# Kernel tuning notes

Hardware: AMD Instinct MI355X
Metric: run time of the kernel (lower is better)

The kernel has to match this reference:

```python
import jax, jax.numpy as jnp
import numpy as np

NQ = 10          # qubits per register
DIM = 2 ** NQ    # 1024 amplitudes
N_CLS = 10       # canonical images (one per class)
N = 16384        # batch of samples
IMG = 28 * 28    # 784 pixels, zero-padded to DIM


def setup_inputs() -> dict:
    key = jax.random.key(0)
    k1, k2, k3 = jax.random.split(key, 3)
    z_re = jax.random.normal(k1, (N, DIM), dtype=jnp.float32)
    z_im = jax.random.normal(k2, (N, DIM), dtype=jnp.float32)
    # inputs are quantum states -> L2-normalize the complex vectors
    nrm = jnp.sqrt(jnp.sum(z_re * z_re + z_im * z_im, axis=1, keepdims=True))
    z_re = z_re / nrm
    z_im = z_im / nrm
    canon = jax.random.uniform(k3, (N_CLS, 1, 28, 28), dtype=jnp.float32)
    return {"z_re": z_re, "z_im": z_im, "canon": canon}


def reference(z_re, z_im, canon):
    # reshape_norm_padding: flatten, zero-pad to 2^nq, L2-normalize (real amplitudes)
    ref = canon.reshape(N_CLS, IMG)
    ref = jnp.pad(ref, ((0, 0), (0, DIM - IMG)))                  # [C, DIM]
    ref = ref / jnp.linalg.norm(ref, axis=1, keepdims=True)
    # Swap test: <Z_anc> = |<val|ref>|^2. ref is real, so with val = z_re + i*z_im:
    #   <val|ref> = (z_re @ ref^T) - i*(z_im @ ref^T)
    s_re = jnp.einsum('nd,cd->nc', z_re, ref)                     # [N, C]
    s_im = jnp.einsum('nd,cd->nc', z_im, ref)                     # [N, C]
    return s_re * s_re + s_im * s_im                              # [N, C] float32
```

## Files before the change

kernel.cpp:

```cpp
#include <hip/hip_runtime.h>

#define NQ    10
#define DIM   1024
#define N_CLS 10
#define NROWS 16384
#define IMG   784

#define ROWS_PER_BLK 8

__device__ __forceinline__ float wave64_sum(float x) {
#define DPP_ADD(ctrl, rmask, bmask)                                           \
  x += __int_as_float(__builtin_amdgcn_update_dpp(                            \
      0, __float_as_int(x), ctrl, rmask, bmask, true));
  DPP_ADD(0x111, 0xf, 0xf)
  DPP_ADD(0x112, 0xf, 0xf)
  DPP_ADD(0x114, 0xf, 0xe)
  DPP_ADD(0x118, 0xf, 0xc)
  DPP_ADD(0x142, 0xa, 0xf)
  DPP_ADD(0x143, 0xc, 0xf)
#undef DPP_ADD
  return x;
}

__global__ void ref_prep_kernel(const float* __restrict__ canon,
                                float* __restrict__ ref) {
  __shared__ float red[256];
  const int c = blockIdx.x;
  const int t = threadIdx.x;
  const float* src = canon + c * IMG;

  float ss = 0.f;
  for (int d = t; d < IMG; d += 256) {
    float v = src[d];
    ss += v * v;
  }
  red[t] = ss;
  __syncthreads();
  for (int s = 128; s > 0; s >>= 1) {
    if (t < s) red[t] += red[t + s];
    __syncthreads();
  }
  const float inv = 1.0f / sqrtf(red[0]);

  for (int d = t; d < DIM; d += 256) {
    ref[c * DIM + d] = (d < IMG) ? src[d] * inv : 0.f;
  }
}

__global__ __launch_bounds__(64, 2) void swaptest_kernel(
    const float* __restrict__ zre, const float* __restrict__ zim,
    const float* __restrict__ ref, float* __restrict__ out) {
  const int lane = threadIdx.x;

  float4 refv[4][N_CLS];
#pragma unroll
  for (int k = 0; k < 4; ++k) {
#pragma unroll
    for (int c = 0; c < N_CLS; ++c) {
      refv[k][c] =
          *(const float4*)(ref + c * DIM + k * 256 + lane * 4);
    }
  }

  const int row0 = blockIdx.x * ROWS_PER_BLK;

  for (int r = 0; r < ROWS_PER_BLK; ++r) {
    const int row = row0 + r;
    if (row >= NROWS) break;

    const float4* pre = (const float4*)(zre + (size_t)row * DIM);
    const float4* pim = (const float4*)(zim + (size_t)row * DIM);

    float4 zr[4], zi[4];
#pragma unroll
    for (int k = 0; k < 4; ++k) {
      zr[k] = pre[k * 64 + lane];
      zi[k] = pim[k * 64 + lane];
    }

    float are[N_CLS], aim[N_CLS];
#pragma unroll
    for (int c = 0; c < N_CLS; ++c) {
      are[c] = 0.f;
      aim[c] = 0.f;
    }

#pragma unroll
    for (int k = 0; k < 4; ++k) {
#pragma unroll
      for (int c = 0; c < N_CLS; ++c) {
        const float4 rv = refv[k][c];
        are[c] += zr[k].x * rv.x + zr[k].y * rv.y + zr[k].z * rv.z +
                  zr[k].w * rv.w;
        aim[c] += zi[k].x * rv.x + zi[k].y * rv.y + zi[k].z * rv.z +
                  zi[k].w * rv.w;
      }
    }

#pragma unroll
    for (int c = 0; c < N_CLS; ++c) {
      are[c] = wave64_sum(are[c]);
      aim[c] = wave64_sum(aim[c]);
    }

    if (lane == 63) {
#pragma unroll
      for (int c = 0; c < N_CLS; ++c) {
        out[(size_t)row * N_CLS + c] = are[c] * are[c] + aim[c] * aim[c];
      }
    }
  }
}

extern "C" void kernel_launch(void* const* d_in, const int* in_sizes, int n_in,
                              void* d_out, int out_size, void* d_ws,
                              size_t ws_size, hipStream_t stream) {
  const float* z_re = (const float*)d_in[0];
  const float* z_im = (const float*)d_in[1];
  const float* canon = (const float*)d_in[2];
  float* out = (float*)d_out;
  float* ref = (float*)d_ws;

  ref_prep_kernel<<<N_CLS, 256, 0, stream>>>(canon, ref);

  const int nblk = NROWS / ROWS_PER_BLK;
  swaptest_kernel<<<nblk, 64, 0, stream>>>(z_re, z_im, ref, out);
}
```

Baseline: 152.0 us.

## Split each row across four waves with shared-memory reduction and row prefetch

Each block now uses four waves that each own a quarter of the 1024 columns, replacing a single wave that covered the whole row. Per-wave partial dot products are combined through shared memory. The next row's float4 is loaded before the current row is computed. The aim is to cut the per-thread register footprint for the reference vectors and get more waves in flight to hide memory latency on this bandwidth-bound kernel, at the cost of two block barriers per row.

```diff
diff --git a/kernel.cpp b/kernel.cpp
--- a/kernel.cpp
+++ b/kernel.cpp
@@ -6,7 +6,8 @@
 #define NROWS 16384
 #define IMG   784
 
-#define ROWS_PER_BLK 8
+#define ROWS_PER_BLK  8
+#define WAVES_PER_BLK 4
 
 __device__ __forceinline__ float wave64_sum(float x) {
 #define DPP_ADD(ctrl, rmask, bmask)                                           \
@@ -47,68 +48,67 @@
   }
 }
 
-__global__ __launch_bounds__(64, 2) void swaptest_kernel(
+__global__ __launch_bounds__(256, 4) void swaptest_kernel(
     const float* __restrict__ zre, const float* __restrict__ zim,
     const float* __restrict__ ref, float* __restrict__ out) {
-  const int lane = threadIdx.x;
+  __shared__ float part[WAVES_PER_BLK][2 * N_CLS];
 
-  float4 refv[4][N_CLS];
+  const int tid = threadIdx.x;
+  const int wave = tid >> 6;
+  const int lane = tid & 63;
+  const int colbase = wave * 256 + lane * 4;
+
+  float4 rv[N_CLS];
 #pragma unroll
-  for (int k = 0; k < 4; ++k) {
+  for (int c = 0; c < N_CLS; ++c)
+    rv[c] = *(const float4*)(ref + c * DIM + colbase);
+
+  const int row0 = blockIdx.x * ROWS_PER_BLK;
+  const float* pre = zre + (size_t)row0 * DIM + colbase;
+  const float* pim = zim + (size_t)row0 * DIM + colbase;
+
+  float4 cre = *(const float4*)pre;
+  float4 cim = *(const float4*)pim;
+
+  for (int r = 0; r < ROWS_PER_BLK; ++r) {
+    float4 nre = cre, nim = cim;
+    if (r + 1 < ROWS_PER_BLK) {
+      nre = *(const float4*)(pre + (size_t)(r + 1) * DIM);
+      nim = *(const float4*)(pim + (size_t)(r + 1) * DIM);
+    }
+
+    float acc[2 * N_CLS];
 #pragma unroll
     for (int c = 0; c < N_CLS; ++c) {
-      refv[k][c] =
-          *(const float4*)(ref + c * DIM + k * 256 + lane * 4);
-    }
-  }
-
-  const int row0 = blockIdx.x * ROWS_PER_BLK;
-
-  for (int r = 0; r < ROWS_PER_BLK; ++r) {
-    const int row = row0 + r;
-    if (row >= NROWS) break;
-
-    const float4* pre = (const float4*)(zre + (size_t)row * DIM);
-    const float4* pim = (const float4*)(zim + (size_t)row * DIM);
-
-    float4 zr[4], zi[4];
-#pragma unroll
-    for (int k = 0; k < 4; ++k) {
-      zr[k] = pre[k * 64 + lane];
-      zi[k] = pim[k * 64 + lane];
-    }
-
-    float are[N_CLS], aim[N_CLS];
-#pragma unroll
-    for (int c = 0; c < N_CLS; ++c) {
-      are[c] = 0.f;
-      aim[c] = 0.f;
+      const float4 rvc = rv[c];
+      acc[2 * c] =
+          cre.x * rvc.x + cre.y * rvc.y + cre.z * rvc.z + cre.w * rvc.w;
+      acc[2 * c + 1] =
+          cim.x * rvc.x + cim.y * rvc.y + cim.z * rvc.z + cim.w * rvc.w;
     }
 
 #pragma unroll
-    for (int k = 0; k < 4; ++k) {
-#pragma unroll
-      for (int c = 0; c < N_CLS; ++c) {
-        const float4 rv = refv[k][c];
-        are[c] += zr[k].x * rv.x + zr[k].y * rv.y + zr[k].z * rv.z +
-                  zr[k].w * rv.w;
-        aim[c] += zi[k].x * rv.x + zi[k].y * rv.y + zi[k].z * rv.z +
-                  zi[k].w * rv.w;
-      }
-    }
-
-#pragma unroll
-    for (int c = 0; c < N_CLS; ++c) {
-      are[c] = wave64_sum(are[c]);
-      aim[c] = wave64_sum(aim[c]);
-    }
+    for (int v = 0; v < 2 * N_CLS; ++v) acc[v] = wave64_sum(acc[v]);
 
     if (lane == 63) {
 #pragma unroll
-      for (int c = 0; c < N_CLS; ++c) {
-        out[(size_t)row * N_CLS + c] = are[c] * are[c] + aim[c] * aim[c];
+      for (int v = 0; v < 2 * N_CLS; ++v) part[wave][v] = acc[v];
+    }
+    __syncthreads();
+
+    if (tid < N_CLS) {
+      float are = 0.f, aim = 0.f;
+#pragma unroll
+      for (int w = 0; w < WAVES_PER_BLK; ++w) {
+        are += part[w][2 * tid];
+        aim += part[w][2 * tid + 1];
       }
+      out[(size_t)(row0 + r) * N_CLS + tid] = are * are + aim * aim;
     }
+    __syncthreads();
+
+    cre = nre;
+    cim = nim;
   }
 }
 
@@ -124,5 +124,5 @@
   ref_prep_kernel<<<N_CLS, 256, 0, stream>>>(canon, ref);
 
   const int nblk = NROWS / ROWS_PER_BLK;
-  swaptest_kernel<<<nblk, 64, 0, stream>>>(z_re, z_im, ref, out);
+  swaptest_kernel<<<nblk, 256, 0, stream>>>(z_re, z_im, ref, out);
 }
```

Measured after the change: 155.1 us. +2.0%, slower.

## Restructure swap-test kernel: lane-per-row dot products with LDS transpose and split-K waves

Applied to the files above, without the earlier changes.

Replaces the one-wave-per-row design, which needed 20 DPP cross-lane reductions per row, with 512-thread blocks over 64 rows. Each of the 8 waves owns a 128-element slice of the dimension, and each lane accumulates full dot products for one row. Coalesced global loads are transposed through XOR-swizzled LDS, the next chunk is prefetched into registers, and ref values are read as wave-uniform (scalar) loads. Partial sums from the waves are combined through LDS at the end. This removes the per-row shuffle reductions and the single-lane stores, at the cost of LDS traffic, two block barriers and higher register pressure.

```diff
diff --git a/kernel.cpp b/kernel.cpp
--- a/kernel.cpp
+++ b/kernel.cpp
@@ -1,26 +1,16 @@
 #include <hip/hip_runtime.h>
 
-#define NQ    10
 #define DIM   1024
 #define N_CLS 10
 #define NROWS 16384
 #define IMG   784
 
-#define ROWS_PER_BLK 8
-
-__device__ __forceinline__ float wave64_sum(float x) {
-#define DPP_ADD(ctrl, rmask, bmask)                                           \
-  x += __int_as_float(__builtin_amdgcn_update_dpp(                            \
-      0, __float_as_int(x), ctrl, rmask, bmask, true));
-  DPP_ADD(0x111, 0xf, 0xf)
-  DPP_ADD(0x112, 0xf, 0xf)
-  DPP_ADD(0x114, 0xf, 0xe)
-  DPP_ADD(0x118, 0xf, 0xc)
-  DPP_ADD(0x142, 0xa, 0xf)
-  DPP_ADD(0x143, 0xc, 0xf)
-#undef DPP_ADD
-  return x;
-}
+#define THREADS 512
+#define WAVES   8
+#define ROWS    64
+#define WIN4    32
+#define CH4     4
+#define NCHUNK  (WIN4 / CH4)
 
 __global__ void ref_prep_kernel(const float* __restrict__ canon,
                                 float* __restrict__ ref) {
@@ -47,68 +37,102 @@
   }
 }
 
-__global__ __launch_bounds__(64, 2) void swaptest_kernel(
+__global__ __launch_bounds__(THREADS, 2) void swaptest_kernel(
     const float* __restrict__ zre, const float* __restrict__ zim,
     const float* __restrict__ ref, float* __restrict__ out) {
-  const int lane = threadIdx.x;
+  __shared__ float4 lds4[WAVES * ROWS * 8];
 
-  float4 refv[4][N_CLS];
+  const int tid  = threadIdx.x;
+  const int lane = tid & 63;
+  const int wv   = __builtin_amdgcn_readfirstlane(tid >> 6);
+  const int row0 = blockIdx.x * ROWS;
+
+  const float4* zre4 = (const float4*)zre;
+  const float4* zim4 = (const float4*)zim;
+  const float4* ref4 = (const float4*)ref;
+
+  float4* sw = lds4 + wv * (ROWS * 8);
+  const int win4 = wv * WIN4;
+
+  const int srow = lane >> 2;
+  const int sgc  = lane & 3;
+  const int sxor = srow & 7;
+
+  float acc[2 * N_CLS];
 #pragma unroll
-  for (int k = 0; k < 4; ++k) {
+  for (int v = 0; v < 2 * N_CLS; ++v) acc[v] = 0.f;
+
+  float4 cre[4], cim[4], nre[4], nim[4];
 #pragma unroll
-    for (int c = 0; c < N_CLS; ++c) {
-      refv[k][c] =
-          *(const float4*)(ref + c * DIM + k * 256 + lane * 4);
+  for (int j = 0; j < 4; ++j) {
+    const int g = (row0 + j * 16 + srow) * (DIM / 4) + win4 + sgc;
+    cre[j] = zre4[g];
+    cim[j] = zim4[g];
+  }
+
+#pragma unroll
+  for (int k = 0; k < NCHUNK; ++k) {
+    if (k + 1 < NCHUNK) {
+#pragma unroll
+      for (int j = 0; j < 4; ++j) {
+        const int g =
+            (row0 + j * 16 + srow) * (DIM / 4) + win4 + (k + 1) * CH4 + sgc;
+        nre[j] = zre4[g];
+        nim[j] = zim4[g];
+      }
+    }
+#pragma unroll
+    for (int j = 0; j < 4; ++j) {
+      const int r8 = (j * 16 + srow) * 8;
+      sw[r8 + (sgc ^ sxor)]       = cre[j];
+      sw[r8 + ((4 + sgc) ^ sxor)] = cim[j];
+    }
+#pragma unroll
+    for (int g = 0; g < CH4; ++g) {
+      const float4 zr = sw[lane * 8 + (g ^ (lane & 7))];
+      const float4 zi = sw[lane * 8 + ((4 + g) ^ (lane & 7))];
+#pragma unroll
+      for (int c = 0; c < N_CLS; ++c) {
+        const float4 rv = ref4[c * (DIM / 4) + win4 + k * CH4 + g];
+        acc[2 * c] = fmaf(
+            zr.w, rv.w,
+            fmaf(zr.z, rv.z, fmaf(zr.y, rv.y, fmaf(zr.x, rv.x, acc[2 * c]))));
+        acc[2 * c + 1] = fmaf(
+            zi.w, rv.w,
+            fmaf(zi.z, rv.z,
+                 fmaf(zi.y, rv.y, fmaf(zi.x, rv.x, acc[2 * c + 1]))));
+      }
+    }
+    if (k + 1 < NCHUNK) {
+#pragma unroll
+      for (int j = 0; j < 4; ++j) {
+        cre[j] = nre[j];
+        cim[j] = nim[j];
+      }
     }
   }
 
-  const int row0 = blockIdx.x * ROWS_PER_BLK;
+  __syncthreads();
+  float* ldsf = (float*)lds4;
+  {
+    float4* pw = (float4*)&ldsf[(wv * 64 + lane) * 20];
+#pragma unroll
+    for (int q = 0; q < 5; ++q)
+      pw[q] = make_float4(acc[4 * q], acc[4 * q + 1], acc[4 * q + 2],
+                          acc[4 * q + 3]);
+  }
+  __syncthreads();
 
-  for (int r = 0; r < ROWS_PER_BLK; ++r) {
-    const int row = row0 + r;
-    if (row >= NROWS) break;
-
-    const float4* pre = (const float4*)(zre + (size_t)row * DIM);
-    const float4* pim = (const float4*)(zim + (size_t)row * DIM);
-
-    float4 zr[4], zi[4];
+  for (int idx = tid; idx < ROWS * N_CLS; idx += THREADS) {
+    const int row = idx / N_CLS;
+    const int c = idx - row * N_CLS;
+    float are = 0.f, aim = 0.f;
 #pragma unroll
-    for (int k = 0; k < 4; ++k) {
-      zr[k] = pre[k * 64 + lane];
-      zi[k] = pim[k * 64 + lane];
+    for (int w = 0; w < WAVES; ++w) {
+      are += ldsf[(w * 64 + row) * 20 + 2 * c];
+      aim += ldsf[(w * 64 + row) * 20 + 2 * c + 1];
     }
-
-    float are[N_CLS], aim[N_CLS];
-#pragma unroll
-    for (int c = 0; c < N_CLS; ++c) {
-      are[c] = 0.f;
-      aim[c] = 0.f;
-    }
-
-#pragma unroll
-    for (int k = 0; k < 4; ++k) {
-#pragma unroll
-      for (int c = 0; c < N_CLS; ++c) {
-        const float4 rv = refv[k][c];
-        are[c] += zr[k].x * rv.x + zr[k].y * rv.y + zr[k].z * rv.z +
-                  zr[k].w * rv.w;
-        aim[c] += zi[k].x * rv.x + zi[k].y * rv.y + zi[k].z * rv.z +
-                  zi[k].w * rv.w;
-      }
-    }
-
-#pragma unroll
-    for (int c = 0; c < N_CLS; ++c) {
-      are[c] = wave64_sum(are[c]);
-      aim[c] = wave64_sum(aim[c]);
-    }
-
-    if (lane == 63) {
-#pragma unroll
-      for (int c = 0; c < N_CLS; ++c) {
-        out[(size_t)row * N_CLS + c] = are[c] * are[c] + aim[c] * aim[c];
-      }
-    }
+    out[(size_t)row0 * N_CLS + idx] = are * are + aim * aim;
   }
 }
 
@@ -123,6 +147,6 @@
 
   ref_prep_kernel<<<N_CLS, 256, 0, stream>>>(canon, ref);
 
-  const int nblk = NROWS / ROWS_PER_BLK;
-  swaptest_kernel<<<nblk, 64, 0, stream>>>(z_re, z_im, ref, out);
+  const int nblk = NROWS / ROWS;
+  swaptest_kernel<<<nblk, THREADS, 0, stream>>>(z_re, z_im, ref, out);
 }
```

After: 165.1 us. 8.6% more time.

## Split each row across 4-lane groups and 4 waves with LDS reduction

Applied to the files above, without the earlier changes.

The kernel moves from 64-thread blocks, where one wave walks 8 rows serially with all reference vectors held in registers, to 256-thread blocks covering 16 rows. Each row's 1024 dimensions are split across four waves and four lanes per wave, and z loads are software-prefetched one step ahead. Reference values are now reloaded from cache on every step instead of being kept in registers. This cuts register pressure and should raise occupancy and memory parallelism. The DPP wave reduction is replaced by partial sums written to shared memory and a final cross-wave sum, at the cost of more reference load traffic and a block-wide barrier.

```diff
diff --git a/kernel.cpp b/kernel.cpp
--- a/kernel.cpp
+++ b/kernel.cpp
@@ -1,26 +1,16 @@
 #include <hip/hip_runtime.h>
 
-#define NQ    10
-#define DIM   1024
-#define N_CLS 10
-#define NROWS 16384
-#define IMG   784
+#define DIM    1024
+#define DIM4   256
+#define N_CLS  10
+#define NROWS  16384
+#define IMG    784
 
-#define ROWS_PER_BLK 8
-
-__device__ __forceinline__ float wave64_sum(float x) {
-#define DPP_ADD(ctrl, rmask, bmask)                                           \
-  x += __int_as_float(__builtin_amdgcn_update_dpp(                            \
-      0, __float_as_int(x), ctrl, rmask, bmask, true));
-  DPP_ADD(0x111, 0xf, 0xf)
-  DPP_ADD(0x112, 0xf, 0xf)
-  DPP_ADD(0x114, 0xf, 0xe)
-  DPP_ADD(0x118, 0xf, 0xc)
-  DPP_ADD(0x142, 0xa, 0xf)
-  DPP_ADD(0x143, 0xc, 0xf)
-#undef DPP_ADD
-  return x;
-}
+#define THREADS  256
+#define WAVES_PB 4
+#define ROWS_PB  16
+#define STEPS    16
+#define PSTRIDE  21
 
 __global__ void ref_prep_kernel(const float* __restrict__ canon,
                                 float* __restrict__ ref) {
@@ -47,68 +37,79 @@
   }
 }
 
-__global__ __launch_bounds__(64, 2) void swaptest_kernel(
+__global__ __launch_bounds__(THREADS, 4) void swaptest_kernel(
     const float* __restrict__ zre, const float* __restrict__ zim,
     const float* __restrict__ ref, float* __restrict__ out) {
-  const int lane = threadIdx.x;
+  __shared__ float part[WAVES_PB * 64 * PSTRIDE];
 
-  float4 refv[4][N_CLS];
+  const int tid  = threadIdx.x;
+  const int lane = tid & 63;
+  const int wv   = tid >> 6;
+  const int q    = lane & 3;
+  const int rloc = lane >> 2;
+
+  const int row = blockIdx.x * ROWS_PB + rloc;
+
+  const float4* zr4 = (const float4*)zre + (size_t)row * DIM4 + wv * 64 + q;
+  const float4* zi4 = (const float4*)zim + (size_t)row * DIM4 + wv * 64 + q;
+  const float4* rf4 = (const float4*)ref + wv * 64 + q;
+
+  float accre[N_CLS], accim[N_CLS];
 #pragma unroll
-  for (int k = 0; k < 4; ++k) {
+  for (int c = 0; c < N_CLS; ++c) {
+    accre[c] = 0.f;
+    accim[c] = 0.f;
+  }
+
+  float4 cre = zr4[0];
+  float4 cim = zi4[0];
+#pragma unroll
+  for (int s = 0; s < STEPS; ++s) {
+    float4 nre, nim;
+    if (s + 1 < STEPS) {
+      nre = zr4[(s + 1) * 4];
+      nim = zi4[(s + 1) * 4];
+    }
 #pragma unroll
     for (int c = 0; c < N_CLS; ++c) {
-      refv[k][c] =
-          *(const float4*)(ref + c * DIM + k * 256 + lane * 4);
+      const float4 rv = rf4[c * DIM4 + s * 4];
+      accre[c] = fmaf(
+          cre.w, rv.w,
+          fmaf(cre.z, rv.z, fmaf(cre.y, rv.y, fmaf(cre.x, rv.x, accre[c]))));
+      accim[c] = fmaf(
+          cim.w, rv.w,
+          fmaf(cim.z, rv.z, fmaf(cim.y, rv.y, fmaf(cim.x, rv.x, accim[c]))));
+    }
+    if (s + 1 < STEPS) {
+      cre = nre;
+      cim = nim;
     }
   }
 
-  const int row0 = blockIdx.x * ROWS_PER_BLK;
-
-  for (int r = 0; r < ROWS_PER_BLK; ++r) {
-    const int row = row0 + r;
-    if (row >= NROWS) break;
-
-    const float4* pre = (const float4*)(zre + (size_t)row * DIM);
-    const float4* pim = (const float4*)(zim + (size_t)row * DIM);
-
-    float4 zr[4], zi[4];
-#pragma unroll
-    for (int k = 0; k < 4; ++k) {
-      zr[k] = pre[k * 64 + lane];
-      zi[k] = pim[k * 64 + lane];
-    }
-
-    float are[N_CLS], aim[N_CLS];
+  {
+    float* pp = &part[(wv * 64 + lane) * PSTRIDE];
 #pragma unroll
     for (int c = 0; c < N_CLS; ++c) {
-      are[c] = 0.f;
-      aim[c] = 0.f;
+      pp[2 * c]     = accre[c];
+      pp[2 * c + 1] = accim[c];
     }
+  }
+  __syncthreads();
 
+  if (tid < ROWS_PB * N_CLS) {
+    const int r = tid / N_CLS;
+    const int c = tid - r * N_CLS;
+    float are = 0.f, aim = 0.f;
 #pragma unroll
-    for (int k = 0; k < 4; ++k) {
+    for (int w = 0; w < WAVES_PB; ++w) {
 #pragma unroll
-      for (int c = 0; c < N_CLS; ++c) {
-        const float4 rv = refv[k][c];
-        are[c] += zr[k].x * rv.x + zr[k].y * rv.y + zr[k].z * rv.z +
-                  zr[k].w * rv.w;
-        aim[c] += zi[k].x * rv.x + zi[k].y * rv.y + zi[k].z * rv.z +
-                  zi[k].w * rv.w;
+      for (int qq = 0; qq < 4; ++qq) {
+        const float* sp = &part[(w * 64 + 4 * r + qq) * PSTRIDE];
+        are += sp[2 * c];
+        aim += sp[2 * c + 1];
       }
     }
-
-#pragma unroll
-    for (int c = 0; c < N_CLS; ++c) {
-      are[c] = wave64_sum(are[c]);
-      aim[c] = wave64_sum(aim[c]);
-    }
-
-    if (lane == 63) {
-#pragma unroll
-      for (int c = 0; c < N_CLS; ++c) {
-        out[(size_t)row * N_CLS + c] = are[c] * are[c] + aim[c] * aim[c];
-      }
-    }
+    out[(size_t)(blockIdx.x * ROWS_PB + r) * N_CLS + c] = are * are + aim * aim;
   }
 }
 
@@ -123,6 +124,6 @@
 
   ref_prep_kernel<<<N_CLS, 256, 0, stream>>>(canon, ref);
 
-  const int nblk = NROWS / ROWS_PER_BLK;
-  swaptest_kernel<<<nblk, 64, 0, stream>>>(z_re, z_im, ref, out);
+  const int nblk = NROWS / ROWS_PB;
+  swaptest_kernel<<<nblk, THREADS, 0, stream>>>(z_re, z_im, ref, out);
 }
```

New measurement: 159.1 us. 1.05x slower.
